# Optimization experiments

Measured on AMD Instinct MI355X. Metric: run time of the kernel, lower is better.

The kernel has to match this reference:

```python
import jax, jax.numpy as jnp
import numpy as np

N_HEADS = 4
N_HIDDEN = 64  # out_features // n_heads
NEG_SLOPE = 0.2


def setup_inputs() -> dict:
    key = jax.random.key(0)
    k1, k2, k3, k4, k5 = jax.random.split(key, 5)
    B, N, F_IN, F_OUT = 1, 4096, 128, 256
    h = jax.random.normal(k1, (B, N, F_IN), dtype=jnp.float32)
    adj_mat = jax.random.uniform(k2, (N, N, 1), dtype=jnp.float32)
    W_proj = jax.random.normal(k3, (F_IN, N_HEADS * N_HIDDEN), dtype=jnp.float32) / np.sqrt(F_IN)
    W_proj_attn = jax.random.normal(k4, (F_IN, N_HEADS * N_HIDDEN // 2), dtype=jnp.float32) / np.sqrt(F_IN)
    w_attn = jax.random.normal(k5, (N_HIDDEN,), dtype=jnp.float32) / np.sqrt(N_HIDDEN)
    return {"h": h, "adj_mat": adj_mat, "W_proj": W_proj, "W_proj_attn": W_proj_attn, "w_attn": w_attn}


def reference(h, adj_mat, W_proj, W_proj_attn, w_attn):
    B, N, _ = h.shape
    H, D = N_HEADS, N_HIDDEN
    half = D // 2
    # value projection: (B, N, H, D)
    g = (h @ W_proj).reshape(B, N, H, D)
    # attention-feature projection: (B, N, H, D//2)
    ga = (h @ W_proj_attn).reshape(B, N, H, half)
    # attn(cat([ga_i, ga_j])) decomposes linearly: e_ij = <w_l, ga_i> + <w_r, ga_j>
    # (identical math to the torch repeat/cat/Linear, without the NxNxD tensor)
    el = jnp.einsum('bnhk,k->bnh', ga, w_attn[:half])   # dest node i term
    er = jnp.einsum('bnhk,k->bnh', ga, w_attn[half:])   # source node j term
    e = jax.nn.leaky_relu(el[:, :, None, :] + er[:, None, :, :], NEG_SLOPE)  # (B, N, N, H)
    mask = adj_mat >= 0.5  # (N, N, 1) broadcasts over (B, N, N, H)
    e = jnp.where(mask, e, -jnp.inf)
    a = jax.nn.softmax(e, axis=2)  # softmax over source nodes j
    # dropout is identity in eval mode
    out = jnp.einsum('bijh,bjhf->bihf', a, g)  # (B, N, H, D)
    return out.reshape(B, N, H * D)  # is_concat=True
```

## Files before the change

### kernel.cpp

```cpp
#include <hip/hip_runtime.h>
#include <hip/hip_bf16.h>

typedef __bf16 bf16_t;
typedef __bf16 bf16x4 __attribute__((ext_vector_type(4)));
typedef __bf16 bf16x8 __attribute__((ext_vector_type(8)));
typedef float floatx2 __attribute__((ext_vector_type(2)));
typedef float floatx4 __attribute__((ext_vector_type(4)));
typedef unsigned int u32;

#define N_NODES 4096
#define F_IN 128
#define NUM_HEADS 4
#define D_HID 64
#define F_OUT 256
#define NEG_SLOPE 0.2f
#define LOG2E 1.4426950408889634f
#define NWORDS 128
#define MASK_BLOCKS 1366
#define PROJ_BLOCKS 512

__global__ __launch_bounds__(384) void prep_kernel(
    const float* __restrict__ adj, u32* __restrict__ maskT,
    const float* __restrict__ hmat, const float* __restrict__ Wp,
    const float* __restrict__ Wa, const float* __restrict__ wattn,
    bf16_t* __restrict__ GB, float* __restrict__ el, float* __restrict__ er)
{
    if (blockIdx.x < MASK_BLOCKS) {
        const int w = blockIdx.x * 384 + threadIdx.x;
        if (w < N_NODES * NWORDS) {
            const float* src = adj + (size_t)w * 32;
            u32 bits = 0;
#pragma unroll
            for (int c = 0; c < 8; ++c) {
                const float4 v = *reinterpret_cast<const float4*>(src + c * 4);
                bits |= (u32)(v.x >= 0.5f) << (4 * c + 0);
                bits |= (u32)(v.y >= 0.5f) << (4 * c + 1);
                bits |= (u32)(v.z >= 0.5f) << (4 * c + 2);
                bits |= (u32)(v.w >= 0.5f) << (4 * c + 3);
            }
            const int row = w >> 7;
            const int jw  = w & 127;
            maskT[(size_t)jw * N_NODES + row] = bits;
        }
        return;
    }
    const int t  = threadIdx.x;
    const int j0 = (blockIdx.x - MASK_BLOCKS) * 8;

    float acc[8] = {0.f, 0.f, 0.f, 0.f, 0.f, 0.f, 0.f, 0.f};

    const float* wptr;
    int stride;
    if (t < 256) { wptr = Wp + t;         stride = 256; }
    else         { wptr = Wa + (t - 256); stride = 128; }

    const float* hbase = hmat + (size_t)j0 * F_IN;

    for (int m = 0; m < F_IN; m += 4) {
        const float w0 = wptr[(size_t)(m + 0) * stride];
        const float w1 = wptr[(size_t)(m + 1) * stride];
        const float w2 = wptr[(size_t)(m + 2) * stride];
        const float w3 = wptr[(size_t)(m + 3) * stride];
#pragma unroll
        for (int jl = 0; jl < 8; ++jl) {
            const float4 hv = *reinterpret_cast<const float4*>(&hbase[jl * F_IN + m]);
            acc[jl] = fmaf(hv.w, w3, fmaf(hv.z, w2, fmaf(hv.y, w1, fmaf(hv.x, w0, acc[jl]))));
        }
    }

    if (t < 256) {
        const int h = t >> 6, f = t & 63;
        bf16x8 o;
#pragma unroll
        for (int q = 0; q < 8; ++q) o[q] = (bf16_t)acc[q];
        const size_t base = ((((size_t)h * 128 + (j0 >> 5)) * 4 + (f >> 4)) * 64
                             + (f & 15) + 16 * ((j0 >> 3) & 3)) * 8;
        *reinterpret_cast<bf16x8*>(&GB[base]) = o;
    } else {
        const int ta = t - 256;
        const int ha = ta >> 5, k = ta & 31;
        const float wl = wattn[k] * LOG2E, wr = wattn[32 + k] * LOG2E;
#pragma unroll
        for (int jl = 0; jl < 8; ++jl) {
            float vl = acc[jl] * wl;
            float vr = acc[jl] * wr;
#pragma unroll
            for (int s = 16; s >= 1; s >>= 1) {
                vl += __shfl_xor(vl, s, 64);
                vr += __shfl_xor(vr, s, 64);
            }
            if (k == 0) {
                el[ha * N_NODES + j0 + jl] = vl;
                er[ha * N_NODES + j0 + jl] = vr;
            }
        }
    }
}

__global__ __launch_bounds__(256, 4) void attn_kernel(
    const u32* __restrict__ maskT, const bf16_t* __restrict__ GB,
    const float* __restrict__ el, const float* __restrict__ er,
    float* __restrict__ numout, float* __restrict__ den_g,
    int ntiles)
{
    const int tid  = threadIdx.x;
    const int wave = tid >> 6;
    const int i0   = blockIdx.x * 128 + wave * 32;
    const int jc   = blockIdx.y;
    const int hh   = blockIdx.z;
    const int lane = tid & 63;
    const int m    = lane & 15;
    const int quad = lane >> 4;
    const int NS   = ntiles * 2;
    const int j32_0 = jc * NS;

    const float el_lo = el[hh * N_NODES + i0 + m];
    const float el_hi = el[hh * N_NODES + i0 + 16 + m];
    const u32*  mTp   = maskT + (size_t)j32_0 * N_NODES + i0 + m;
    const float* erp  = er + hh * N_NODES + j32_0 * 32 + quad * 8;
    const bf16_t* gb  = GB + (size_t)hh * (128 * 4 * 512)
                           + (size_t)j32_0 * 2048 + lane * 8;

    floatx4 accL0 = {0.f, 0.f, 0.f, 0.f};
    floatx4 accL1 = accL0, accL2 = accL0, accL3 = accL0, accdL = accL0;
    floatx4 accH0 = accL0, accH1 = accL0, accH2 = accL0, accH3 = accL0, accdH = accL0;
    bf16x8 ones;
#pragma unroll
    for (int q = 0; q < 8; ++q) ones[q] = (bf16_t)1.0f;

    u32 mLc = mTp[0], mHc = mTp[16];
    float4 e0c = *reinterpret_cast<const float4*>(erp);
    float4 e1c = *reinterpret_cast<const float4*>(erp + 4);
    bf16x8 b0c = *reinterpret_cast<const bf16x8*>(gb);
    bf16x8 b1c = *reinterpret_cast<const bf16x8*>(gb + 512);
    bf16x8 b2c = *reinterpret_cast<const bf16x8*>(gb + 1024);
    bf16x8 b3c = *reinterpret_cast<const bf16x8*>(gb + 1536);

    for (int s = 0; s < NS; ++s) {
        const int d = (s + 1 < NS) ? 1 : 0;
        const u32    mLn = mTp[(size_t)d * N_NODES];
        const u32    mHn = mTp[(size_t)d * N_NODES + 16];
        const float4 e0n = *reinterpret_cast<const float4*>(erp + d * 32);
        const float4 e1n = *reinterpret_cast<const float4*>(erp + d * 32 + 4);
        const bf16_t* gpn = gb + (size_t)d * 2048;
        const bf16x8 b0n = *reinterpret_cast<const bf16x8*>(gpn);
        const bf16x8 b1n = *reinterpret_cast<const bf16x8*>(gpn + 512);
        const bf16x8 b2n = *reinterpret_cast<const bf16x8*>(gpn + 1024);
        const bf16x8 b3n = *reinterpret_cast<const bf16x8*>(gpn + 1536);

        const u32 byL = (mLc >> (quad * 8)) & 0xffu;
        const u32 byH = (mHc >> (quad * 8)) & 0xffu;
        const floatx2 evp[4] = {{e0c.x, e0c.y}, {e0c.z, e0c.w},
                                {e1c.x, e1c.y}, {e1c.z, e1c.w}};
        const floatx2 eL2 = {el_lo, el_lo};
        const floatx2 eH2 = {el_hi, el_hi};

        bf16x8 afL, afH;
#pragma unroll
        for (int qp = 0; qp < 4; ++qp) {
            floatx2 sL = eL2 + evp[qp];
            floatx2 sH = eH2 + evp[qp];
            sL = __builtin_elementwise_max(sL, sL * NEG_SLOPE);
            sH = __builtin_elementwise_max(sH, sH * NEG_SLOPE);
            const float pL0 = ((byL >> (2 * qp))     & 1u) ? __builtin_amdgcn_exp2f(sL.x) : 0.f;
            const float pL1 = ((byL >> (2 * qp + 1)) & 1u) ? __builtin_amdgcn_exp2f(sL.y) : 0.f;
            const float pH0 = ((byH >> (2 * qp))     & 1u) ? __builtin_amdgcn_exp2f(sH.x) : 0.f;
            const float pH1 = ((byH >> (2 * qp + 1)) & 1u) ? __builtin_amdgcn_exp2f(sH.y) : 0.f;
            afL[2 * qp]     = (bf16_t)pL0;
            afL[2 * qp + 1] = (bf16_t)pL1;
            afH[2 * qp]     = (bf16_t)pH0;
            afH[2 * qp + 1] = (bf16_t)pH1;
        }

        accdL = __builtin_amdgcn_mfma_f32_16x16x32_bf16(afL, ones, accdL, 0, 0, 0);
        accdH = __builtin_amdgcn_mfma_f32_16x16x32_bf16(afH, ones, accdH, 0, 0, 0);

        accL0 = __builtin_amdgcn_mfma_f32_16x16x32_bf16(afL, b0c, accL0, 0, 0, 0);
        accH0 = __builtin_amdgcn_mfma_f32_16x16x32_bf16(afH, b0c, accH0, 0, 0, 0);
        accL1 = __builtin_amdgcn_mfma_f32_16x16x32_bf16(afL, b1c, accL1, 0, 0, 0);
        accH1 = __builtin_amdgcn_mfma_f32_16x16x32_bf16(afH, b1c, accH1, 0, 0, 0);
        accL2 = __builtin_amdgcn_mfma_f32_16x16x32_bf16(afL, b2c, accL2, 0, 0, 0);
        accH2 = __builtin_amdgcn_mfma_f32_16x16x32_bf16(afH, b2c, accH2, 0, 0, 0);
        accL3 = __builtin_amdgcn_mfma_f32_16x16x32_bf16(afL, b3c, accL3, 0, 0, 0);
        accH3 = __builtin_amdgcn_mfma_f32_16x16x32_bf16(afH, b3c, accH3, 0, 0, 0);

        mLc = mLn; mHc = mHn; e0c = e0n; e1c = e1n;
        b0c = b0n; b1c = b1n; b2c = b2n; b3c = b3n;
        mTp += N_NODES;
        erp += 32;
        gb  += 2048;
    }

    float* nrow = numout + (size_t)jc * ((size_t)N_NODES * F_OUT);
    const int ibL = i0 + quad * 4;
    const int ibH = ibL + 16;
#pragma unroll
    for (int r = 0; r < 4; ++r) {
        float* dL = nrow + (size_t)(ibL + r) * F_OUT + hh * D_HID + m;
        dL[0]  = accL0[r];
        dL[16] = accL1[r];
        dL[32] = accL2[r];
        dL[48] = accL3[r];
        float* dH = nrow + (size_t)(ibH + r) * F_OUT + hh * D_HID + m;
        dH[0]  = accH0[r];
        dH[16] = accH1[r];
        dH[32] = accH2[r];
        dH[48] = accH3[r];
    }
    if (m == 0) {
#pragma unroll
        for (int r = 0; r < 4; ++r) {
            den_g[((size_t)jc * N_NODES + ibL + r) * NUM_HEADS + hh] = accdL[r];
            den_g[((size_t)jc * N_NODES + ibH + r) * NUM_HEADS + hh] = accdH[r];
        }
    }
}

template<int NJC>
__global__ __launch_bounds__(256) void reduce_kernel(
    const float* __restrict__ num, const float* __restrict__ den,
    float* __restrict__ out)
{
    const int t4   = blockIdx.x * 256 + threadIdx.x;
    const int base = t4 * 4;
    const int i  = base >> 8;
    const int hh = (base & 255) >> 6;
    float4 n = {0.f, 0.f, 0.f, 0.f};
    float d = 0.f;
#pragma unroll
    for (int jc = 0; jc < NJC; ++jc) {
        const float4 v = *reinterpret_cast<const float4*>(
            num + (size_t)jc * ((size_t)N_NODES * F_OUT) + base);
        n.x += v.x; n.y += v.y; n.z += v.z; n.w += v.w;
        d += den[((size_t)jc * N_NODES + i) * NUM_HEADS + hh];
    }
    const float rd = 1.0f / d;
    float4 o = {n.x * rd, n.y * rd, n.z * rd, n.w * rd};
    *reinterpret_cast<float4*>(out + base) = o;
}

extern "C" void kernel_launch(void* const* d_in, const int* in_sizes, int n_in,
                              void* d_out, int out_size, void* d_ws, size_t ws_size,
                              hipStream_t stream)
{
    const float* hmat = (const float*)d_in[0];
    const float* adj  = (const float*)d_in[1];
    const float* Wp   = (const float*)d_in[2];
    const float* Wa   = (const float*)d_in[3];
    const float* watt = (const float*)d_in[4];
    float* out = (float*)d_out;

    char* ws = (char*)d_ws;
    bf16_t* GB   = (bf16_t*)ws;
    float*  el   = (float*)(ws + (2ull << 20));
    float*  er   = (float*)(ws + (2ull << 20) + (64ull << 10));
    u32*    mskT = (u32*)(ws + (2ull << 20) + (128ull << 10));
    const size_t baseoff = (4ull << 20) + (128ull << 10);

    const size_t num_bytes = (size_t)N_NODES * F_OUT * 4;
    const size_t den_bytes = (size_t)N_NODES * NUM_HEADS * 4;
    const int njc = (ws_size >= baseoff + 8 * (num_bytes + den_bytes)) ? 8
                  : (ws_size >= baseoff + 4 * (num_bytes + den_bytes)) ? 4 : 2;

    float* num = (float*)(ws + baseoff);
    float* den = (float*)(ws + baseoff + (size_t)njc * num_bytes);

    prep_kernel<<<MASK_BLOCKS + PROJ_BLOCKS, 384, 0, stream>>>(
        adj, mskT, hmat, Wp, Wa, watt, GB, el, er);
    attn_kernel<<<dim3(32, njc, NUM_HEADS), 256, 0, stream>>>(
        mskT, GB, el, er, num, den, (N_NODES / njc) / 64);
    if (njc == 8)      reduce_kernel<8><<<(N_NODES * F_OUT) / 1024, 256, 0, stream>>>(num, den, out);
    else if (njc == 4) reduce_kernel<4><<<(N_NODES * F_OUT) / 1024, 256, 0, stream>>>(num, den, out);
    else               reduce_kernel<2><<<(N_NODES * F_OUT) / 1024, 256, 0, stream>>>(num, den, out);
}
```

Baseline: 161.7 us.

## Split prep into mask and projection kernels, transpose mask through LDS

The fused prep kernel is split into a dedicated mask kernel and a projection kernel. The mask kernel packs 64 rows x 4 words per block and transposes them through shared memory, so stores to the transposed bitmask become coalesced runs of 64 consecutive words instead of writes strided by N_NODES. The cost is an extra kernel launch, and the mask and projection work no longer run concurrently within one launch.

```diff
diff --git a/kernel.cpp b/kernel.cpp
--- a/kernel.cpp
+++ b/kernel.cpp
@@ -16,36 +16,40 @@
 #define NEG_SLOPE 0.2f
 #define LOG2E 1.4426950408889634f
 #define NWORDS 128
-#define MASK_BLOCKS 1366
-#define PROJ_BLOCKS 512
-
-__global__ __launch_bounds__(384) void prep_kernel(
-    const float* __restrict__ adj, u32* __restrict__ maskT,
+
+__global__ __launch_bounds__(256) void mask_kernel(
+    const float* __restrict__ adj, u32* __restrict__ maskT)
+{
+    __shared__ u32 lds[4 * 65];
+    const int t   = threadIdx.x;
+    const int r0  = (blockIdx.x & 63) * 64;
+    const int jw0 = (blockIdx.x >> 6) * 4;
+    const int row = r0 + (t >> 2);
+    const int jw  = jw0 + (t & 3);
+
+    const float* src = adj + (size_t)row * N_NODES + jw * 32;
+    u32 bits = 0;
+#pragma unroll
+    for (int c = 0; c < 8; ++c) {
+        const float4 v = *reinterpret_cast<const float4*>(src + c * 4);
+        bits |= (u32)(v.x >= 0.5f) << (4 * c + 0);
+        bits |= (u32)(v.y >= 0.5f) << (4 * c + 1);
+        bits |= (u32)(v.z >= 0.5f) << (4 * c + 2);
+        bits |= (u32)(v.w >= 0.5f) << (4 * c + 3);
+    }
+    lds[(t & 3) * 65 + (t >> 2)] = bits;
+    __syncthreads();
+    const int w = t >> 6, l = t & 63;
+    maskT[(size_t)(jw0 + w) * N_NODES + r0 + l] = lds[w * 65 + l];
+}
+
+__global__ __launch_bounds__(384) void proj_kernel(
     const float* __restrict__ hmat, const float* __restrict__ Wp,
     const float* __restrict__ Wa, const float* __restrict__ wattn,
     bf16_t* __restrict__ GB, float* __restrict__ el, float* __restrict__ er)
 {
-    if (blockIdx.x < MASK_BLOCKS) {
-        const int w = blockIdx.x * 384 + threadIdx.x;
-        if (w < N_NODES * NWORDS) {
-            const float* src = adj + (size_t)w * 32;
-            u32 bits = 0;
-#pragma unroll
-            for (int c = 0; c < 8; ++c) {
-                const float4 v = *reinterpret_cast<const float4*>(src + c * 4);
-                bits |= (u32)(v.x >= 0.5f) << (4 * c + 0);
-                bits |= (u32)(v.y >= 0.5f) << (4 * c + 1);
-                bits |= (u32)(v.z >= 0.5f) << (4 * c + 2);
-                bits |= (u32)(v.w >= 0.5f) << (4 * c + 3);
-            }
-            const int row = w >> 7;
-            const int jw  = w & 127;
-            maskT[(size_t)jw * N_NODES + row] = bits;
-        }
-        return;
-    }
-    const int t  = threadIdx.x;
-    const int j0 = (blockIdx.x - MASK_BLOCKS) * 8;
+    const int t = threadIdx.x;
+    const int j0 = blockIdx.x * 8;
 
     float acc[8] = {0.f, 0.f, 0.f, 0.f, 0.f, 0.f, 0.f, 0.f};
 
@@ -265,8 +269,8 @@
     float* num = (float*)(ws + baseoff);
     float* den = (float*)(ws + baseoff + (size_t)njc * num_bytes);
 
-    prep_kernel<<<MASK_BLOCKS + PROJ_BLOCKS, 384, 0, stream>>>(
-        adj, mskT, hmat, Wp, Wa, watt, GB, el, er);
+    mask_kernel<<<64 * (NWORDS / 4), 256, 0, stream>>>(adj, mskT);
+    proj_kernel<<<512, 384, 0, stream>>>(hmat, Wp, Wa, watt, GB, el, er);
     attn_kernel<<<dim3(32, njc, NUM_HEADS), 256, 0, stream>>>(
         mskT, GB, el, er, num, den, (N_NODES / njc) / 64);
     if (njc == 8)      reduce_kernel<8><<<(N_NODES * F_OUT) / 1024, 256, 0, stream>>>(num, den, out);
```

Measured after the change: 162.6 us. Within noise of the previous version (+0.6%).
